# Kernel optimization log

Measured on AMD Instinct MI355X. Metric: run time of the kernel, lower is better.

The kernel has to match this reference:

```python
import jax, jax.numpy as jnp
import numpy as np

B, C, L, MID, HID, OUT, K = 4096, 6, 1024, 512, 512, 256, 5
EPS = 1e-5


def _bn_eval(x, g, b, m, v):
    # BatchNorm1d eval mode on (B, C, T): normalize per channel with running stats
    inv = g / jnp.sqrt(v + EPS)
    return (x - m[None, :, None]) * inv[None, :, None] + b[None, :, None]


def setup_inputs() -> dict:
    key = jax.random.key(0)
    ks = jax.random.split(key, 12)
    s_in = 1.0 / np.sqrt(L)
    s_hid = 1.0 / np.sqrt(HID)
    inp = {
        "x": jax.random.normal(ks[0], (B, C, L), jnp.float32),
        # k stacked self-attention branches (two Linear(L, MID) each)
        "aW1": jax.random.normal(ks[1], (K, L, MID), jnp.float32) * s_in,
        "ab1": jnp.zeros((K, MID), jnp.float32),
        "aW2": jax.random.normal(ks[2], (K, L, MID), jnp.float32) * s_in,
        "ab2": jnp.zeros((K, MID), jnp.float32),
        # linearExchangeLayer: Linear(K*C, C)
        "linW": jax.random.normal(ks[3], (K * C, C), jnp.float32) / np.sqrt(K * C),
        "linb": jnp.zeros((C,), jnp.float32),
        # GraphConvolution weights
        "gW1": jax.random.normal(ks[4], (L, HID), jnp.float32) * s_in,
        "gb1": jnp.zeros((HID,), jnp.float32),
        "gW2": jax.random.normal(ks[5], (HID, OUT), jnp.float32) * s_hid,
        "gb2": jnp.zeros((OUT,), jnp.float32),
        # PReLU (single shared parameter, torch default 0.25)
        "prelu_a": jnp.array(0.25, jnp.float32),
        # BatchNorm1d params + running stats (eval mode)
        "bn1_g": jnp.ones((C,), jnp.float32),
        "bn1_b": jnp.zeros((C,), jnp.float32),
        "bn1_m": jnp.zeros((C,), jnp.float32),
        "bn1_v": jnp.ones((C,), jnp.float32),
        "bn2_g": jnp.ones((C,), jnp.float32),
        "bn2_b": jnp.zeros((C,), jnp.float32),
        "bn2_m": jnp.zeros((C,), jnp.float32),
        "bn2_v": jnp.ones((C,), jnp.float32),
    }
    return inp


def reference(x, aW1, ab1, aW2, ab2, linW, linb, gW1, gb1, gW2, gb2,
              prelu_a, bn1_g, bn1_b, bn1_m, bn1_v, bn2_g, bn2_b, bn2_m, bn2_v):
    b, c, l = x.shape
    k = aW1.shape[0]
    # --- multi-head attention adjacency: (b, c, c) ---
    q = jnp.einsum('bcl,klm->bkcm', x, aW1) + ab1[None, :, None, :]
    kv = jnp.einsum('bcl,klm->bkcm', x, aW2) + ab2[None, :, None, :]
    scores = jax.nn.softmax(jnp.einsum('bkcm,bkdm->bkcd', q, kv), axis=-1)
    # concat heads along last dim: (b, c, k*c)
    cat = scores.transpose(0, 2, 1, 3).reshape(b, c, k * c)
    A = jax.nn.softmax(cat @ linW + linb, axis=-1)  # (b, c, c)
    # --- GraphConvolution 1 (dropout identity in eval) ---
    h = jnp.einsum('bcd,bdh->bch', A, x @ gW1) + gb1
    # PReLU then BatchNorm1d
    h = jnp.where(h >= 0, h, prelu_a * h)
    h = _bn_eval(h, bn1_g, bn1_b, bn1_m, bn1_v)
    # --- GraphConvolution 2 ---
    out = jnp.einsum('bcd,bdh->bch', A, h @ gW2) + gb2
    out = _bn_eval(out, bn2_g, bn2_b, bn2_m, bn2_v)
    return out
```

## Files before the change

### kernel.cpp

```cpp
#include <hip/hip_runtime.h>
#include <hip/hip_bf16.h>


using bf16 = __hip_bfloat16;
using s16x8 = __attribute__((ext_vector_type(8))) short;
using f32x4 = __attribute__((ext_vector_type(4))) float;

#define AS1(p) ((__attribute__((address_space(1))) void*)((void*)(p)))
#define AS3(p) ((__attribute__((address_space(3))) void*)(p))

#if defined(__has_builtin)
#if __has_builtin(__builtin_amdgcn_global_load_lds)
#define HAVE_GLL 1
#endif
#endif

__device__ __forceinline__ float s2f(short s) {
  union { unsigned int u; float f; } c;
  c.u = ((unsigned int)(unsigned short)s) << 16;
  return c.f;
}
__device__ __forceinline__ short f2s(float x) {
  bf16 b = __float2bfloat16(x);
  short s;
  __builtin_memcpy(&s, &b, 2);
  return s;
}

__global__ void cvt_f32_bf16(const float* __restrict__ in, bf16* __restrict__ out, int n8) {
  int i = blockIdx.x * blockDim.x + threadIdx.x;
  if (i >= n8) return;
  float4 p0 = ((const float4*)in)[i * 2];
  float4 p1 = ((const float4*)in)[i * 2 + 1];
  s16x8 v;
  v[0] = f2s(p0.x); v[1] = f2s(p0.y); v[2] = f2s(p0.z); v[3] = f2s(p0.w);
  v[4] = f2s(p1.x); v[5] = f2s(p1.y); v[6] = f2s(p1.z); v[7] = f2s(p1.w);
  ((s16x8*)out)[i] = v;
}

__global__ void transpose_f2b(const float* __restrict__ in, bf16* __restrict__ out,
                              int R, int C) {
  __shared__ short tile[32][33];
  const float* src = in + (size_t)blockIdx.z * R * C;
  short* dst = (short*)out + (size_t)blockIdx.z * R * C;
  int r0 = blockIdx.x * 32, c0 = blockIdx.y * 32;
  int tx = threadIdx.x, ty = threadIdx.y;
#pragma unroll
  for (int i = 0; i < 4; ++i)
    tile[ty + i * 8][tx] = f2s(src[(size_t)(r0 + ty + i * 8) * C + c0 + tx]);
  __syncthreads();
#pragma unroll
  for (int i = 0; i < 4; ++i)
    dst[(size_t)(c0 + ty + i * 8) * R + r0 + tx] = tile[tx][ty + i * 8];
}

template <int AF32>
__global__ __launch_bounds__(256) void gemm_bt(
    const void* __restrict__ Ag,
    const bf16* __restrict__ Bt0, const bf16* __restrict__ Bt1,
    const float* __restrict__ bias0, const float* __restrict__ bias1, int boff,
    bf16* __restrict__ out0, bf16* __restrict__ out1,
    int M, int N, int K) {
  const bf16* Bt = (blockIdx.z == 0) ? Bt0 : Bt1;
  const float* bias = (blockIdx.z == 0) ? bias0 : bias1;
  bf16* Cg = (blockIdx.z == 0) ? out0 : out1;

  __shared__ short lA[128 * 32];
  __shared__ short lB[128 * 32];

  const int tid = threadIdx.x;
  const int lane = tid & 63, w = tid >> 6;
  const int wr = w >> 1, wc = w & 1;
  const int l16 = lane & 15, quad = lane >> 4;
  const int lrow = lane >> 2;
  const int scol = (((lane & 3) ^ ((lane >> 3) & 3)) * 8);

  const size_t rm0 = (size_t)blockIdx.x * 128;
  const size_t cn0 = (size_t)blockIdx.y * 128;

  f32x4 acc[4][4];
#pragma unroll
  for (int i = 0; i < 4; ++i)
#pragma unroll
    for (int j = 0; j < 4; ++j) acc[i][j] = (f32x4){0.f, 0.f, 0.f, 0.f};

  for (int kb = 0; kb < K; kb += 32) {
#pragma unroll
    for (int t = 0; t < 2; ++t) {
      int chunk = w * 2 + t;
      int row = chunk * 16 + lrow;
      const bf16* gb = Bt + (cn0 + row) * (size_t)K + kb + scol;
#ifdef HAVE_GLL
      __builtin_amdgcn_global_load_lds(AS1(gb), AS3(lB + chunk * 512), 16, 0, 0);
#else
      *(s16x8*)(lB + chunk * 512 + lane * 8) = *(const s16x8*)gb;
#endif
      if (AF32) {
        const float* ga = (const float*)Ag + (rm0 + row) * (size_t)K + kb + scol;
        float4 p0 = *(const float4*)ga;
        float4 p1 = *(const float4*)(ga + 4);
        s16x8 v;
        v[0] = f2s(p0.x); v[1] = f2s(p0.y); v[2] = f2s(p0.z); v[3] = f2s(p0.w);
        v[4] = f2s(p1.x); v[5] = f2s(p1.y); v[6] = f2s(p1.z); v[7] = f2s(p1.w);
        *(s16x8*)(lA + chunk * 512 + lane * 8) = v;
      } else {
        const bf16* ga = (const bf16*)Ag + (rm0 + row) * (size_t)K + kb + scol;
#ifdef HAVE_GLL
        __builtin_amdgcn_global_load_lds(AS1(ga), AS3(lA + chunk * 512), 16, 0, 0);
#else
        *(s16x8*)(lA + chunk * 512 + lane * 8) = *(const s16x8*)ga;
#endif
      }
    }
    __syncthreads();

    const int q2 = (quad ^ ((l16 >> 1) & 3)) * 8;
    s16x8 af[4], bfv[4];
#pragma unroll
    for (int i = 0; i < 4; ++i) {
      af[i] = *(const s16x8*)(lA + (wr * 64 + i * 16 + l16) * 32 + q2);
      bfv[i] = *(const s16x8*)(lB + (wc * 64 + i * 16 + l16) * 32 + q2);
    }
#pragma unroll
    for (int i = 0; i < 4; ++i)
#pragma unroll
      for (int j = 0; j < 4; ++j)
        acc[i][j] = __builtin_amdgcn_mfma_f32_16x16x32_bf16(af[i], bfv[j], acc[i][j], 0, 0, 0);
    __syncthreads();
  }

#pragma unroll
  for (int j = 0; j < 4; ++j) {
    size_t col = cn0 + wc * 64 + j * 16 + l16;
    float bv = bias ? bias[boff + col] : 0.f;
#pragma unroll
    for (int i = 0; i < 4; ++i) {
      size_t rowb = rm0 + wr * 64 + i * 16 + quad * 4;
#pragma unroll
      for (int r = 0; r < 4; ++r) {
        float v = acc[i][j][r] + bv;
        Cg[(rowb + r) * (size_t)N + col] = __float2bfloat16(v);
      }
    }
  }
}

__global__ __launch_bounds__(256) void scores_mfma(
    const bf16* __restrict__ Q, const bf16* __restrict__ KV,
    float* __restrict__ S, int head) {
  const int tid = threadIdx.x;
  const int lane = tid & 63, w = tid >> 6;
  const int l16 = lane & 15, quad = lane >> 4;
  const int b0 = (blockIdx.x * 4 + w) * 2;

  int gr = (l16 < 8) ? (b0 * 6 + l16) : ((b0 + 1) * 6 + (l16 - 8));
  if (gr > 24575) gr = 24575;

  const short* qrow = (const short*)Q + (size_t)gr * 512 + quad * 8;
  const short* krow = (const short*)KV + (size_t)gr * 512 + quad * 8;

  f32x4 acc = (f32x4){0.f, 0.f, 0.f, 0.f};
#pragma unroll
  for (int kk = 0; kk < 16; ++kk) {
    s16x8 a = *(const s16x8*)(qrow + kk * 32);
    s16x8 b = *(const s16x8*)(krow + kk * 32);
    acc = __builtin_amdgcn_mfma_f32_16x16x32_bf16(a, b, acc, 0, 0, 0);
  }

  if (l16 < 6) {
#pragma unroll
    for (int r = 0; r < 4; ++r) {
      int m = quad * 4 + r;
      if (m < 6)
        S[((size_t)b0 * 5 + head) * 36 + m * 6 + l16] = acc[r];
    }
  } else if (l16 >= 8 && l16 < 14) {
#pragma unroll
    for (int r = 0; r < 4; ++r) {
      int m = quad * 4 + r;
      if (m >= 8 && m < 14)
        S[((size_t)(b0 + 1) * 5 + head) * 36 + (m - 8) * 6 + (l16 - 8)] = acc[r];
    }
  }
}

__global__ void batch_mid_kernel(const float* __restrict__ S, const bf16* __restrict__ XG,
                                 const float* __restrict__ linW, const float* __restrict__ linb,
                                 const float* __restrict__ gb1, const float* __restrict__ prelu,
                                 const float* __restrict__ g1, const float* __restrict__ b1,
                                 const float* __restrict__ m1, const float* __restrict__ v1,
                                 float* __restrict__ Afull, bf16* __restrict__ H) {
  int b = blockIdx.x, tid = threadIdx.x;
  __shared__ float p[5][6][6];
  __shared__ float Ar[6][6];
  __shared__ float lw[30][6];
  __shared__ float lbv[6];
  __shared__ float sc1[6], sm1[6], sb1[6];

  if (tid < 30) {
    int k = tid / 6, c = tid % 6;
    const float* sp = S + ((size_t)b * 5 + k) * 36 + c * 6;
    float v[6], mx = sp[0];
#pragma unroll
    for (int d = 0; d < 6; ++d) { v[d] = sp[d]; mx = fmaxf(mx, v[d]); }
    float s = 0.f;
#pragma unroll
    for (int d = 0; d < 6; ++d) { v[d] = expf(v[d] - mx); s += v[d]; }
    float inv = 1.f / s;
#pragma unroll
    for (int d = 0; d < 6; ++d) p[k][c][d] = v[d] * inv;
#pragma unroll
    for (int j = 0; j < 6; ++j) lw[tid][j] = linW[tid * 6 + j];
  }
  if (tid < 6) {
    lbv[tid] = linb[tid];
    sc1[tid] = g1[tid] * rsqrtf(v1[tid] + 1e-5f);
    sm1[tid] = m1[tid];
    sb1[tid] = b1[tid];
  }
  __syncthreads();

  if (tid < 6) {
    int c = tid;
    float ap[6];
#pragma unroll
    for (int j = 0; j < 6; ++j) ap[j] = lbv[j];
    for (int k = 0; k < 5; ++k)
#pragma unroll
      for (int d = 0; d < 6; ++d) {
        float pv = p[k][c][d];
#pragma unroll
        for (int j = 0; j < 6; ++j) ap[j] += pv * lw[k * 6 + d][j];
      }
    float mx = ap[0];
#pragma unroll
    for (int j = 1; j < 6; ++j) mx = fmaxf(mx, ap[j]);
    float s = 0.f;
#pragma unroll
    for (int j = 0; j < 6; ++j) { ap[j] = expf(ap[j] - mx); s += ap[j]; }
    float inv = 1.f / s;
#pragma unroll
    for (int j = 0; j < 6; ++j) {
      float a = ap[j] * inv;
      Ar[c][j] = a;
      Afull[(size_t)b * 36 + c * 6 + j] = a;
    }
  }
  __syncthreads();

  float pa = prelu[0];
  for (int col = tid; col < 512; col += 64) {
    float xg[6];
#pragma unroll
    for (int d = 0; d < 6; ++d) xg[d] = s2f(((const short*)XG)[((size_t)b * 6 + d) * 512 + col]);
    float gbv = gb1[col];
#pragma unroll
    for (int c = 0; c < 6; ++c) {
      float h = gbv;
#pragma unroll
      for (int d = 0; d < 6; ++d) h += Ar[c][d] * xg[d];
      h = (h >= 0.f) ? h : pa * h;
      h = (h - sm1[c]) * sc1[c] + sb1[c];
      H[((size_t)b * 6 + c) * 512 + col] = __float2bfloat16(h);
    }
  }
}

__global__ void batch_out_kernel(const float* __restrict__ Afull, const bf16* __restrict__ HW,
                                 const float* __restrict__ gb2,
                                 const float* __restrict__ g2, const float* __restrict__ b2,
                                 const float* __restrict__ m2, const float* __restrict__ v2,
                                 float* __restrict__ out) {
  int b = blockIdx.x, tid = threadIdx.x;
  __shared__ float Ar[36];
  __shared__ float sc[6], sm[6], sb[6];
  if (tid < 36) Ar[tid] = Afull[(size_t)b * 36 + tid];
  if (tid < 6) {
    sc[tid] = g2[tid] * rsqrtf(v2[tid] + 1e-5f);
    sm[tid] = m2[tid];
    sb[tid] = b2[tid];
  }
  __syncthreads();
  for (int col = tid; col < 256; col += 64) {
    float hw[6];
#pragma unroll
    for (int d = 0; d < 6; ++d) hw[d] = s2f(((const short*)HW)[((size_t)b * 6 + d) * 256 + col]);
    float gv = gb2[col];
#pragma unroll
    for (int c = 0; c < 6; ++c) {
      float o = gv;
#pragma unroll
      for (int d = 0; d < 6; ++d) o += Ar[c * 6 + d] * hw[d];
      o = (o - sm[c]) * sc[c] + sb[c];
      out[((size_t)b * 6 + c) * 256 + col] = o;
    }
  }
}

extern "C" void kernel_launch(void* const* d_in, const int* in_sizes, int n_in,
                              void* d_out, int out_size, void* d_ws, size_t ws_size,
                              hipStream_t stream) {
  const float* x    = (const float*)d_in[0];
  const float* aW1  = (const float*)d_in[1];
  const float* ab1  = (const float*)d_in[2];
  const float* aW2  = (const float*)d_in[3];
  const float* ab2  = (const float*)d_in[4];
  const float* linW = (const float*)d_in[5];
  const float* linb = (const float*)d_in[6];
  const float* gW1  = (const float*)d_in[7];
  const float* gb1  = (const float*)d_in[8];
  const float* gW2  = (const float*)d_in[9];
  const float* gb2  = (const float*)d_in[10];
  const float* prelu = (const float*)d_in[11];
  const float* bn1g = (const float*)d_in[12];
  const float* bn1b = (const float*)d_in[13];
  const float* bn1m = (const float*)d_in[14];
  const float* bn1v = (const float*)d_in[15];
  const float* bn2g = (const float*)d_in[16];
  const float* bn2b = (const float*)d_in[17];
  const float* bn2m = (const float*)d_in[18];
  const float* bn2v = (const float*)d_in[19];

  char* ws = (char*)d_ws;
  bf16* W1T  = (bf16*)(ws + 0);
  bf16* W2T  = (bf16*)(ws + 5242880);
  bf16* G1T  = (bf16*)(ws + 10485760);
  bf16* G2T  = (bf16*)(ws + 11534336);
  float* S   = (float*)(ws + 11796480);
  float* Af  = (float*)(ws + 14745600);
  bf16* BufA = (bf16*)(ws + 15335424);
  bf16* BufB = (bf16*)(ws + 40501248);
  bf16* Xb   = (bf16*)(ws + 65667072);
  const bool big = ws_size >= 115998720ull;

  dim3 tb(32, 8);
  transpose_f2b<<<dim3(32, 16, 5), tb, 0, stream>>>(aW1, W1T, 1024, 512);
  transpose_f2b<<<dim3(32, 16, 5), tb, 0, stream>>>(aW2, W2T, 1024, 512);
  transpose_f2b<<<dim3(32, 16, 1), tb, 0, stream>>>(gW1, G1T, 1024, 512);
  transpose_f2b<<<dim3(16, 8, 1),  tb, 0, stream>>>(gW2, G2T, 512, 256);
  if (big) cvt_f32_bf16<<<12288, 256, 0, stream>>>(x, Xb, 3145728);

  for (int k = 0; k < 5; ++k) {
    const bf16* w1 = W1T + (size_t)k * 512 * 1024;
    const bf16* w2 = W2T + (size_t)k * 512 * 1024;
    if (big)
      gemm_bt<0><<<dim3(192, 4, 2), 256, 0, stream>>>(
          Xb, w1, w2, ab1, ab2, k * 512, BufA, BufB, 24576, 512, 1024);
    else
      gemm_bt<1><<<dim3(192, 4, 2), 256, 0, stream>>>(
          x, w1, w2, ab1, ab2, k * 512, BufA, BufB, 24576, 512, 1024);
    scores_mfma<<<512, 256, 0, stream>>>(BufA, BufB, S, k);
  }

  if (big)
    gemm_bt<0><<<dim3(192, 4, 1), 256, 0, stream>>>(
        Xb, G1T, G1T, nullptr, nullptr, 0, BufA, BufA, 24576, 512, 1024);
  else
    gemm_bt<1><<<dim3(192, 4, 1), 256, 0, stream>>>(
        x, G1T, G1T, nullptr, nullptr, 0, BufA, BufA, 24576, 512, 1024);

  batch_mid_kernel<<<4096, 64, 0, stream>>>(S, BufA, linW, linb, gb1, prelu,
                                            bn1g, bn1b, bn1m, bn1v, Af, BufB);

  gemm_bt<0><<<dim3(192, 2, 1), 256, 0, stream>>>(
      BufB, G2T, G2T, nullptr, nullptr, 0, BufA, BufA, 24576, 256, 512);

  batch_out_kernel<<<4096, 64, 0, stream>>>(Af, BufA, gb2, bn2g, bn2b, bn2m, bn2v,
                                            (float*)d_out);
}
```

Before: 734.9 us.

## Add 256x256-tile 8-wave GEMM with phased LDS double-buffer pipeline

Adds a new bf16 MFMA GEMM that uses 256x256 output tiles, 512 threads and a double-buffered 128KB LDS staging area. Each K-step is split into four phases that interleave global-to-LDS loads with MFMA quadrants, with explicit barriers, waitcnts and setprio. The larger tile is meant to raise arithmetic intensity and hide memory latency for the attention-projection and graph-convolution GEMMs. In exchange, each block holds far more registers and LDS, so occupancy drops, and the grid becomes much smaller (192 blocks or fewer).

Measured after the change: 678.5 us. 1.08x faster.

```diff
diff --git a/kernel.cpp b/kernel.cpp
--- a/kernel.cpp
+++ b/kernel.cpp
@@ -145,6 +145,171 @@
   }
 }
 
+__global__ __launch_bounds__(512, 2) void gemm256_8ph(
+    const bf16* __restrict__ A,
+    const bf16* __restrict__ Bt0, const bf16* __restrict__ Bt1,
+    const float* __restrict__ bias0, const float* __restrict__ bias1, int boff,
+    bf16* __restrict__ out0, bf16* __restrict__ out1,
+    int M, int N, int K) {
+  const bf16* Bt = (blockIdx.z == 0) ? Bt0 : Bt1;
+  const float* bias = (blockIdx.z == 0) ? bias0 : bias1;
+  bf16* Cg = (blockIdx.z == 0) ? out0 : out1;
+
+  __shared__ __attribute__((aligned(16))) short ldsS[65536];
+
+  const int tid = threadIdx.x;
+  const int w = tid >> 6, l = tid & 63;
+  const int l16 = l & 15, quad = l >> 4;
+  const int wr = w >> 2, wc = w & 3;
+
+  const size_t rm0 = (size_t)blockIdx.x * 256;
+  const size_t cn0 = (size_t)blockIdx.y * 256;
+
+  const int colS = ((l & 7) ^ (l >> 3)) * 8;
+  const int rowS = w * 16 + (l >> 3);
+  const short* pAs = (const short*)A + (rm0 + rowS) * (size_t)K + colS;
+  const short* pBs = (const short*)Bt + (cn0 + rowS) * (size_t)K + colS;
+
+  const int u0 = (quad ^ (l16 & 7)) * 8;
+  const int u1 = ((quad + 4) ^ (l16 & 7)) * 8;
+
+  f32x4 acc[8][4];
+#pragma unroll
+  for (int i = 0; i < 8; ++i)
+#pragma unroll
+    for (int j = 0; j < 4; ++j) acc[i][j] = (f32x4){0.f, 0.f, 0.f, 0.f};
+
+  s16x8 af[4][2], bf0[2][2], bf1[2][2];
+
+  const int T = K >> 6;
+
+#ifdef HAVE_GLL
+#define SA(BUF, H, KB) do {                                                          \
+    __builtin_amdgcn_global_load_lds(AS1(pAs + (size_t)((H) * 128) * K + (KB)),      \
+        AS3(ldsS + (BUF) * 32768 + (H) * 8192 + w * 1024), 16, 0, 0);                \
+    __builtin_amdgcn_global_load_lds(AS1(pAs + (size_t)((H) * 128 + 8) * K + (KB)),  \
+        AS3(ldsS + (BUF) * 32768 + (H) * 8192 + w * 1024 + 512), 16, 0, 0);          \
+  } while (0)
+#define SB(BUF, H, KB) do {                                                          \
+    __builtin_amdgcn_global_load_lds(AS1(pBs + (size_t)((H) * 128) * K + (KB)),      \
+        AS3(ldsS + (BUF) * 32768 + 16384 + (H) * 8192 + w * 1024), 16, 0, 0);        \
+    __builtin_amdgcn_global_load_lds(AS1(pBs + (size_t)((H) * 128 + 8) * K + (KB)),  \
+        AS3(ldsS + (BUF) * 32768 + 16384 + (H) * 8192 + w * 1024 + 512), 16, 0, 0);  \
+  } while (0)
+#else
+#define SA(BUF, H, KB) do {                                                          \
+    *(s16x8*)(ldsS + (BUF) * 32768 + (H) * 8192 + w * 1024 + l * 8) =                \
+        *(const s16x8*)(pAs + (size_t)((H) * 128) * K + (KB));                       \
+    *(s16x8*)(ldsS + (BUF) * 32768 + (H) * 8192 + w * 1024 + 512 + l * 8) =          \
+        *(const s16x8*)(pAs + (size_t)((H) * 128 + 8) * K + (KB));                   \
+  } while (0)
+#define SB(BUF, H, KB) do {                                                          \
+    *(s16x8*)(ldsS + (BUF) * 32768 + 16384 + (H) * 8192 + w * 1024 + l * 8) =        \
+        *(const s16x8*)(pBs + (size_t)((H) * 128) * K + (KB));                       \
+    *(s16x8*)(ldsS + (BUF) * 32768 + 16384 + (H) * 8192 + w * 1024 + 512 + l * 8) =  \
+        *(const s16x8*)(pBs + (size_t)((H) * 128 + 8) * K + (KB));                   \
+  } while (0)
+#endif
+
+#define LDA(BUF, MH) do {                                                            \
+    _Pragma("unroll") for (int i = 0; i < 4; ++i) {                                  \
+      const short* bse = ldsS + (BUF) * 32768 + wr * 8192 + (MH) * 4096 +            \
+                         i * 1024 + l16 * 64;                                        \
+      af[i][0] = *(const s16x8*)(bse + u0);                                          \
+      af[i][1] = *(const s16x8*)(bse + u1);                                          \
+    }                                                                                \
+  } while (0)
+
+#define LDB(BUF, NH, DST) do {                                                       \
+    _Pragma("unroll") for (int n = 0; n < 2; ++n) {                                  \
+      const short* bse = ldsS + (BUF) * 32768 + 16384 + (wc >> 1) * 8192 +           \
+                         (wc & 1) * 4096 + (NH) * 2048 + n * 1024 + l16 * 64;        \
+      DST[n][0] = *(const s16x8*)(bse + u0);                                         \
+      DST[n][1] = *(const s16x8*)(bse + u1);                                         \
+    }                                                                                \
+  } while (0)
+
+#define MFMAQ(MH, NH, BSET) do {                                                     \
+    _Pragma("unroll") for (int i = 0; i < 4; ++i)                                    \
+      _Pragma("unroll") for (int n = 0; n < 2; ++n) {                                \
+        acc[(MH) * 4 + i][(NH) * 2 + n] = __builtin_amdgcn_mfma_f32_16x16x32_bf16(   \
+            af[i][0], BSET[n][0], acc[(MH) * 4 + i][(NH) * 2 + n], 0, 0, 0);         \
+        acc[(MH) * 4 + i][(NH) * 2 + n] = __builtin_amdgcn_mfma_f32_16x16x32_bf16(   \
+            af[i][1], BSET[n][1], acc[(MH) * 4 + i][(NH) * 2 + n], 0, 0, 0);         \
+      }                                                                              \
+  } while (0)
+
+#define BARX() asm volatile("s_barrier" ::: "memory")
+#define LGKM0() do { asm volatile("s_waitcnt lgkmcnt(0)" ::: "memory");              \
+                     __builtin_amdgcn_sched_barrier(0); } while (0)
+#define VM6() do { asm volatile("s_waitcnt vmcnt(6)" ::: "memory");                  \
+                   __builtin_amdgcn_sched_barrier(0); } while (0)
+
+#define TILE_STEP(BUF, t) do {                                                       \
+    const int kN_ = ((t) + 1 < T ? (t) + 1 : T - 1) << 6;                            \
+    const int k2_ = ((t) + 2 < T ? (t) + 2 : T - 1) << 6;                            \
+               \
+    LDA(BUF, 0); LDB(BUF, 0, bf0); LDB(BUF, 1, bf1);                                 \
+    SA((BUF) ^ 1, 1, kN_);                                                           \
+    BARX(); LGKM0();                                                                 \
+    __builtin_amdgcn_s_setprio(1); MFMAQ(0, 0, bf0); __builtin_amdgcn_s_setprio(0);  \
+    BARX();                                                                          \
+                        \
+    SB(BUF, 0, k2_);                                                                 \
+    BARX();                                                                          \
+    __builtin_amdgcn_s_setprio(1); MFMAQ(0, 1, bf1); __builtin_amdgcn_s_setprio(0);  \
+    BARX();                                                                          \
+                                               \
+    LDA(BUF, 1);                                                                     \
+    SB(BUF, 1, k2_);                                                                 \
+    BARX(); LGKM0();                                                                 \
+    __builtin_amdgcn_s_setprio(1); MFMAQ(1, 1, bf1); __builtin_amdgcn_s_setprio(0);  \
+    BARX();                                                                          \
+                         \
+    SA(BUF, 0, k2_);                                                                 \
+    VM6();                                                                           \
+    BARX();                                                                          \
+    __builtin_amdgcn_s_setprio(1); MFMAQ(1, 0, bf0); __builtin_amdgcn_s_setprio(0);  \
+    BARX();                                                                          \
+  } while (0)
+
+  {
+    const int k1_ = (T > 1 ? 1 : 0) << 6;
+    SB(0, 0, 0); SB(0, 1, 0); SA(0, 0, 0); SA(0, 1, 0);
+    SB(1, 0, k1_); SB(1, 1, k1_); SA(1, 0, k1_);
+    VM6();
+    BARX();
+  }
+
+  for (int t = 0; t < T; t += 2) {
+    TILE_STEP(0, t);
+    TILE_STEP(1, t + 1);
+  }
+
+#pragma unroll
+  for (int j = 0; j < 4; ++j) {
+    size_t col = cn0 + wc * 64 + j * 16 + l16;
+    float bv = bias ? bias[boff + col] : 0.f;
+#pragma unroll
+    for (int i = 0; i < 8; ++i) {
+      size_t rowb = rm0 + wr * 128 + i * 16 + quad * 4;
+#pragma unroll
+      for (int r = 0; r < 4; ++r) {
+        Cg[(rowb + r) * (size_t)N + col] = __float2bfloat16(acc[i][j][r] + bv);
+      }
+    }
+  }
+#undef SA
+#undef SB
+#undef LDA
+#undef LDB
+#undef MFMAQ
+#undef BARX
+#undef LGKM0
+#undef VM6
+#undef TILE_STEP
+}
+
 __global__ __launch_bounds__(256) void scores_mfma(
     const bf16* __restrict__ Q, const bf16* __restrict__ KV,
     float* __restrict__ S, int head) {
@@ -344,7 +509,7 @@
     const bf16* w1 = W1T + (size_t)k * 512 * 1024;
     const bf16* w2 = W2T + (size_t)k * 512 * 1024;
     if (big)
-      gemm_bt<0><<<dim3(192, 4, 2), 256, 0, stream>>>(
+      gemm256_8ph<<<dim3(96, 2, 2), 512, 0, stream>>>(
           Xb, w1, w2, ab1, ab2, k * 512, BufA, BufB, 24576, 512, 1024);
     else
       gemm_bt<1><<<dim3(192, 4, 2), 256, 0, stream>>>(
@@ -353,7 +518,7 @@
   }
 
   if (big)
-    gemm_bt<0><<<dim3(192, 4, 1), 256, 0, stream>>>(
+    gemm256_8ph<<<dim3(96, 2, 1), 512, 0, stream>>>(
         Xb, G1T, G1T, nullptr, nullptr, 0, BufA, BufA, 24576, 512, 1024);
   else
     gemm_bt<1><<<dim3(192, 4, 1), 256, 0, stream>>>(
@@ -362,8 +527,12 @@
   batch_mid_kernel<<<4096, 64, 0, stream>>>(S, BufA, linW, linb, gb1, prelu,
                                             bn1g, bn1b, bn1m, bn1v, Af, BufB);
 
-  gemm_bt<0><<<dim3(192, 2, 1), 256, 0, stream>>>(
-      BufB, G2T, G2T, nullptr, nullptr, 0, BufA, BufA, 24576, 256, 512);
+  if (big)
+    gemm256_8ph<<<dim3(96, 1, 1), 512, 0, stream>>>(
+        BufB, G2T, G2T, nullptr, nullptr, 0, BufA, BufA, 24576, 256, 512);
+  else
+    gemm_bt<0><<<dim3(192, 2, 1), 256, 0, stream>>>(
+        BufB, G2T, G2T, nullptr, nullptr, 0, BufA, BufA, 24576, 256, 512);
 
   batch_out_kernel<<<4096, 64, 0, stream>>>(Af, BufA, gb2, bn2g, bn2b, bn2m, bn2v,
                                             (float*)d_out);
```
